# Performance work log

Measured on AMD Instinct MI355X. Metric: run time of the kernel, lower is better.

The kernel has to match this reference:

```python
import jax, jax.numpy as jnp
import numpy as np

B, NA, T, NV, D = 24, 50, 10, 196, 512


def setup_inputs() -> dict:
    key = jax.random.key(0)
    k1, k2 = jax.random.split(key)
    return {
        "audio_feats": jax.random.normal(k1, (B, NA, D), dtype=jnp.float32),
        "visual_feats": jax.random.normal(k2, (B, T, NV, D), dtype=jnp.float32),
        "temperature": jnp.float32(2.5),
        "scale_factor": jnp.float32(2.5),
        "threshold": jnp.float32(-2.5),
    }


def _l2norm(x):
    # F.normalize(dim=-1): x / max(||x||, 1e-12)
    n = jnp.sqrt(jnp.sum(x * x, axis=-1, keepdims=True))
    return x / jnp.maximum(n, 1e-12)


def reference(audio_feats, visual_feats, temperature, scale_factor, threshold):
    b = audio_feats.shape[0]
    a = _l2norm(audio_feats)          # (B,Na,D)
    v = _l2norm(visual_feats)         # (B,T,Nv,D)
    # all-pairs token similarities: (B,B,Na,T,Nv)
    sims = jnp.einsum('xad,ytvd->xyatv', a, v) / temperature

    # aggregate_temporal_similarities
    th = jax.nn.sigmoid(threshold)
    max_vis = jnp.max(sims, axis=-1)            # (B,B,Na,T)
    raw_diff = max_vis - th
    sel = jax.nn.relu(raw_diff) * scale_factor  # selection strength
    weighted_sum = jnp.sum(max_vis * sel, axis=-1)   # over T
    weights_sum = jnp.sum(sel, axis=-1)
    token_sims = weighted_sum / jnp.maximum(weights_sum, 1e-6)
    clip_sims = jnp.mean(token_sims, axis=-1)   # (B,B)
    fraction_selected = jnp.mean((raw_diff > 0).astype(jnp.float32))

    # InfoNCE
    idx = jnp.arange(b)
    losses_a2v = -jax.nn.log_softmax(clip_sims, axis=1)[idx, idx]
    losses_v2a = -jax.nn.log_softmax(clip_sims.T, axis=1)[idx, idx]
    contrastive_loss = jnp.mean(losses_a2v + losses_v2a) / 2

    # regularization
    neg = jnp.clip(sims, -20.0, 0.0)
    l_nonneg = jnp.mean(neg * neg)
    temp_low = jnp.maximum(-jnp.log(temperature), 0.0) ** 2   # log(1)=0
    temp_high = jnp.maximum(jnp.log(temperature) - jnp.log(4.0), 0.0) ** 2
    l_cal = temp_low + temp_high
    l_threshold = jnp.maximum(th - 0.9, 0.0) ** 2 + jnp.maximum(0.1 - th, 0.0) ** 2
    l_scale = jnp.maximum(scale_factor - 20.0, 0.0) ** 2 + jnp.maximum(1.0 - scale_factor, 0.0) ** 2
    reg_loss = 0.15 * l_nonneg + 2.0 * l_cal + 0.1 * l_threshold + 0.1 * l_scale

    # selection reward on positive pairs (diagonal)
    pos_diffs = raw_diff[idx, idx]                       # (B,Na,T)
    sel_ratio = (jnp.tanh(20.0 * pos_diffs) + 1.0) / 2.0
    selection_reward = -0.1 * jnp.log1p(jnp.mean(sel_ratio))

    total_loss = selection_reward + contrastive_loss + reg_loss
    return (total_loss, contrastive_loss, reg_loss, fraction_selected, selection_reward)
```

## Files before the change

### kernel.cpp

```cpp
#include <hip/hip_runtime.h>
#include <math.h>

#define B_   24
#define NA_  50
#define T_   10
#define NV_  196
#define D_   512
#define M_   1200
#define MPAD 1280
#define NVP  224
#define YT_  240
#define VROWS (YT_ * NVP)
#define ABLK 320

#define NT    16
#define BUFB  32768u
#define VBASE 16384u

typedef __bf16 bf16x8 __attribute__((ext_vector_type(8)));
typedef float  f32x4  __attribute__((ext_vector_type(4)));
typedef unsigned short ushort8 __attribute__((ext_vector_type(8)));

__device__ __forceinline__ unsigned short f2bf(float f) {
    unsigned u = __float_as_uint(f);
    u += 0x7FFF + ((u >> 16) & 1);
    return (unsigned short)(u >> 16);
}

__device__ __forceinline__ void gload16(const void* g, void* l) {
    __builtin_amdgcn_global_load_lds(
        (const __attribute__((address_space(1))) unsigned int*)g,
        (__attribute__((address_space(3))) unsigned int*)l, 16, 0, 0);
}

__global__ void normconv_kernel(const float* __restrict__ a,
                                const float* __restrict__ vf,
                                const float* __restrict__ tempPtr,
                                unsigned short* __restrict__ Abf,
                                unsigned short* __restrict__ Vbf,
                                float* __restrict__ accs) {
    if (blockIdx.x == 0 && threadIdx.x < 4) accs[threadIdx.x] = 0.0f;
    int w = threadIdx.x >> 6, lane = threadIdx.x & 63;
    int bid = blockIdx.x;
    const float* src = nullptr;
    ushort8* dst;
    float tscale = 1.0f;
    if (bid < ABLK) {
        int row = bid * 4 + w;
        dst = (ushort8*)(Abf + (size_t)row * D_ + lane * 8);
        if (row < M_) { src = a + (size_t)row * D_ + lane * 8; tscale = tempPtr[0]; }
    } else {
        int row = (bid - ABLK) * 4 + w;
        dst = (ushort8*)(Vbf + (size_t)row * D_ + lane * 8);
        int yt = row / NVP, vv = row - yt * NVP;
        if (vv < NV_) src = vf + ((size_t)yt * NV_ + vv) * D_ + lane * 8;
    }
    if (src) {
        float4 u = *(const float4*)src;
        float4 v = *(const float4*)(src + 4);
        float s = u.x*u.x + u.y*u.y + u.z*u.z + u.w*u.w
                + v.x*v.x + v.y*v.y + v.z*v.z + v.w*v.w;
        #pragma unroll
        for (int off = 32; off; off >>= 1) s += __shfl_xor(s, off, 64);
        float sc = 1.0f / (fmaxf(sqrtf(s), 1e-12f) * tscale);
        ushort8 o;
        o[0]=f2bf(u.x*sc); o[1]=f2bf(u.y*sc); o[2]=f2bf(u.z*sc); o[3]=f2bf(u.w*sc);
        o[4]=f2bf(v.x*sc); o[5]=f2bf(v.y*sc); o[6]=f2bf(v.z*sc); o[7]=f2bf(v.w*sc);
        *dst = o;
    } else {
        ushort8 z = (ushort8)0;
        *dst = z;
    }
}

#define RD_FRAGS(AF, BV, BASE)                                                  \
    _Pragma("unroll") for (int i = 0; i < 4; ++i)                               \
        AF[i] = *(const bf16x8*)((BASE) + aoff[i]);                             \
    _Pragma("unroll") for (int j = 0; j < 7; ++j)                               \
        BV[j] = *(const bf16x8*)((BASE) + boff[j]);

#define MFMA_ALL(AF, BV)                                                        \
    _Pragma("unroll") for (int i = 0; i < 4; ++i)                               \
        _Pragma("unroll") for (int j = 0; j < 7; ++j)                           \
            acc[i][j] = __builtin_amdgcn_mfma_f32_16x16x32_bf16(AF[i], BV[j], acc[i][j], 0, 0, 0);

#define STAGE_T(T, BASEOFF)                                                     \
    _Pragma("unroll") for (int k = 0; k < 4; ++k)                               \
        gload16(gp[k] + (T) * 32, (void*)(lds + (BASEOFF) + loff[k]));

__global__ __launch_bounds__(512, 1) void simred_kernel(
    const unsigned short* __restrict__ Abf, const unsigned short* __restrict__ Vbf,
    float* __restrict__ maxvis, float* __restrict__ accNonneg)
{
    __shared__ __align__(16) unsigned char lds[2 * BUFB];
    float* maxredp = (float*)(lds + 30720);
    float* redbufp = (float*)(lds + BUFB + 30720);

    const int tid  = threadIdx.x;
    const int lane = tid & 63;
    const int w    = tid >> 6;
    const int lrow = lane >> 2;
    const int lcol = lane & 3;
    const int q    = lane >> 4;
    const int m16  = lane & 15;
    const int wr   = w & 3;
    const int wc   = w >> 2;

    const int lin = blockIdx.y * gridDim.x + blockIdx.x;
    const int swz = (lin & 7) * 150 + (lin >> 3);
    const int bx  = swz % 5;
    const int yt  = swz / 5;
    const int rowA0 = bx * 256;
    const size_t vRow0 = (size_t)yt * NVP;

    const int scol = lcol ^ ((lrow >> 1) & 3);
    const unsigned short* gp[4];
    unsigned loff[4];
    #pragma unroll
    for (int k = 0; k < 4; ++k) {
        int u = w + 8 * k;
        if (u < 16)      gp[k] = Abf + ((size_t)(rowA0 + u * 16 + lrow)) * D_ + scol * 8;
        else if (u < 30) gp[k] = Vbf + (vRow0 + (size_t)((u - 16) * 16 + lrow)) * D_ + scol * 8;
        else             gp[k] = Abf + (size_t)lane * 8;
        loff[k] = (unsigned)u * 1024u;
    }

    const unsigned rsw = (unsigned)((m16 >> 1) & 3) * 16u;
    unsigned aoff[4], boff[7];
    #pragma unroll
    for (int i = 0; i < 4; ++i)
        aoff[i] = (unsigned)(wr * 64 + i * 16 + m16) * 64u + (((unsigned)q * 16u) ^ rsw);
    #pragma unroll
    for (int j = 0; j < 7; ++j)
        boff[j] = VBASE + (unsigned)(wc * 112 + j * 16 + m16) * 64u + (((unsigned)q * 16u) ^ rsw);

    f32x4 acc[4][7];
    #pragma unroll
    for (int i = 0; i < 4; ++i)
        #pragma unroll
        for (int j = 0; j < 7; ++j) acc[i][j] = (f32x4)0.0f;

    bf16x8 afA[4], bvA[7], afB[4], bvB[7];

    STAGE_T(0, 0u)
    STAGE_T(1, BUFB)
    asm volatile("s_waitcnt vmcnt(4)\ns_barrier" ::: "memory");
    RD_FRAGS(afA, bvA, lds)

    #pragma unroll
    for (int tp = 0; tp < 8; ++tp) {
        const int t = 2 * tp;
        asm volatile("s_waitcnt vmcnt(0) lgkmcnt(0)\ns_barrier" ::: "memory");
        if (t + 2 < NT) { STAGE_T(t + 2, 0u) }
        RD_FRAGS(afB, bvB, lds + BUFB)
        __builtin_amdgcn_s_setprio(1);
        MFMA_ALL(afA, bvA)
        __builtin_amdgcn_s_setprio(0);
        asm volatile("s_waitcnt vmcnt(0) lgkmcnt(0)\ns_barrier" ::: "memory");
        if (t + 3 < NT) { STAGE_T(t + 3, BUFB) }
        if (t + 2 < NT) { RD_FRAGS(afA, bvA, lds) }
        __builtin_amdgcn_s_setprio(1);
        MFMA_ALL(afB, bvB)
        __builtin_amdgcn_s_setprio(0);
    }

    float cs = 0.0f;
    #pragma unroll
    for (int i = 0; i < 4; ++i)
        #pragma unroll
        for (int j = 0; j < 7; ++j)
            #pragma unroll
            for (int r = 0; r < 4; ++r) {
                float v = acc[i][j][r];
                float cv = fminf(fmaxf(v, -20.0f), 0.0f);
                cs += cv * cv;
            }
    #pragma unroll
    for (int off = 32; off; off >>= 1) cs += __shfl_xor(cs, off, 64);
    if (lane == 0) redbufp[w] = cs;

    bool colv[7];
    #pragma unroll
    for (int j = 0; j < 7; ++j) colv[j] = (wc * 112 + j * 16 + m16) < NV_;
    #pragma unroll
    for (int i = 0; i < 4; ++i) {
        float mx[4] = {-3e38f, -3e38f, -3e38f, -3e38f};
        #pragma unroll
        for (int j = 0; j < 7; ++j)
            #pragma unroll
            for (int r = 0; r < 4; ++r)
                mx[r] = fmaxf(mx[r], colv[j] ? acc[i][j][r] : -3e38f);
        #pragma unroll
        for (int r = 0; r < 4; ++r) {
            float mm = mx[r];
            #pragma unroll
            for (int off = 1; off <= 8; off <<= 1) mm = fmaxf(mm, __shfl_xor(mm, off, 64));
            if (m16 == 0) maxredp[wc * 256 + wr * 64 + i * 16 + q * 4 + r] = mm;
        }
    }
    __syncthreads();
    if (tid == 0) atomicAdd(accNonneg, redbufp[0] + redbufp[1] + redbufp[2] + redbufp[3]
                                     + redbufp[4] + redbufp[5] + redbufp[6] + redbufp[7]);
    if (tid < 256) {
        float mm = fmaxf(maxredp[tid], maxredp[256 + tid]);
        int R = rowA0 + tid;
        if (R < M_) {
            int x = R / NA_, a = R - x * NA_;
            int y = yt / T_, t = yt - y * T_;
            maxvis[(((size_t)x * B_ + y) * NA_ + a) * T_ + t] = mm;
        }
    }
}

__global__ void aggfin_kernel(const float* __restrict__ maxvis,
                              const float* __restrict__ thrPtr,
                              const float* __restrict__ scalePtr,
                              const float* __restrict__ tempPtr,
                              float* __restrict__ clipSims,
                              float* __restrict__ accs,
                              float* __restrict__ out)
{
    int xy = blockIdx.x;
    int x = xy / B_, y = xy % B_;
    int a = threadIdx.x;
    float th    = 1.0f / (1.0f + expf(-thrPtr[0]));
    float scale = scalePtr[0];
    float token = 0.0f, cnt = 0.0f, selsum = 0.0f;
    if (a < NA_) {
        const float* p = maxvis + (((size_t)x * B_ + y) * NA_ + a) * T_;
        float ws = 0.0f, ss = 0.0f;
        #pragma unroll
        for (int t = 0; t < T_; ++t) {
            float mv  = p[t];
            float rd  = mv - th;
            float sel = fmaxf(rd, 0.0f) * scale;
            ws += mv * sel;
            ss += sel;
            if (rd > 0.0f) cnt += 1.0f;
            if (x == y) selsum += 0.5f * (tanhf(20.0f * rd) + 1.0f);
        }
        token = ws / fmaxf(ss, 1e-6f);
    }
    #pragma unroll
    for (int off = 32; off; off >>= 1) {
        token  += __shfl_xor(token,  off, 64);
        cnt    += __shfl_xor(cnt,    off, 64);
        selsum += __shfl_xor(selsum, off, 64);
    }
    if (threadIdx.x == 0) {
        clipSims[x * B_ + y] = token / (float)NA_;
        atomicAdd(&accs[1], cnt);
        if (x == y) atomicAdd(&accs[2], selsum);
    }
    __threadfence();
    unsigned last = 0;
    if (threadIdx.x == 0) {
        unsigned v = atomicAdd((unsigned int*)(accs + 3), 1u);
        last = ((v % (unsigned)(B_ * B_)) == (unsigned)(B_ * B_ - 1));
    }
    last = __shfl((int)last, 0, 64);
    if (!last) return;
    __threadfence();

    __shared__ float cs[B_ * B_];
    int tid = threadIdx.x;
    for (int i = tid; i < B_ * B_; i += 64) cs[i] = clipSims[i];
    __syncthreads();
    float lsum = 0.0f;
    if (tid < B_) {
        int i = tid;
        float m = -1e30f;
        for (int j = 0; j < B_; ++j) m = fmaxf(m, cs[i * B_ + j]);
        float e = 0.0f;
        for (int j = 0; j < B_; ++j) e += expf(cs[i * B_ + j] - m);
        float la = m + logf(e) - cs[i * B_ + i];
        float m2 = -1e30f;
        for (int j = 0; j < B_; ++j) m2 = fmaxf(m2, cs[j * B_ + i]);
        float e2 = 0.0f;
        for (int j = 0; j < B_; ++j) e2 += expf(cs[j * B_ + i] - m2);
        float lv = m2 + logf(e2) - cs[i * B_ + i];
        lsum = la + lv;
    }
    #pragma unroll
    for (int off = 32; off; off >>= 1) lsum += __shfl_xor(lsum, off, 64);
    if (tid == 0) {
        float contrastive = lsum / (float)B_ * 0.5f;
        float temp = tempPtr[0], scl = scalePtr[0];
        float th2 = 1.0f / (1.0f + expf(-thrPtr[0]));
        float l_nonneg = accs[0] / 56448000.0f;
        float logt = logf(temp);
        float tl  = fmaxf(-logt, 0.0f);
        float thi = fmaxf(logt - logf(4.0f), 0.0f);
        float l_cal = tl * tl + thi * thi;
        float t1 = fmaxf(th2 - 0.9f, 0.0f), t2 = fmaxf(0.1f - th2, 0.0f);
        float l_thr = t1 * t1 + t2 * t2;
        float s1 = fmaxf(scl - 20.0f, 0.0f), s2 = fmaxf(1.0f - scl, 0.0f);
        float l_scale = s1 * s1 + s2 * s2;
        float reg = 0.15f * l_nonneg + 2.0f * l_cal + 0.1f * l_thr + 0.1f * l_scale;
        float frac   = accs[1] / 288000.0f;
        float selrew = -0.1f * log1pf(accs[2] / 12000.0f);
        out[0] = selrew + contrastive + reg;
        out[1] = contrastive;
        out[2] = reg;
        out[3] = frac;
        out[4] = selrew;
    }
}

extern "C" void kernel_launch(void* const* d_in, const int* in_sizes, int n_in,
                              void* d_out, int out_size, void* d_ws, size_t ws_size,
                              hipStream_t stream) {
    const float* audio  = (const float*)d_in[0];
    const float* visual = (const float*)d_in[1];
    const float* temp   = (const float*)d_in[2];
    const float* scale  = (const float*)d_in[3];
    const float* thr    = (const float*)d_in[4];
    float* out = (float*)d_out;

    unsigned char* wsb = (unsigned char*)d_ws;
    unsigned short* Abf = (unsigned short*)wsb;
    unsigned short* Vbf = (unsigned short*)(wsb + 1310720);
    float* maxvis   = (float*)(wsb + 1310720 + 55050240);
    float* clipSims = (float*)(wsb + 1310720 + 55050240 + 1152000);
    float* accs     = clipSims + 576;

    normconv_kernel<<<ABLK + VROWS / 4, 256, 0, stream>>>(audio, visual, temp, Abf, Vbf, accs);

    dim3 grid(MPAD / 256, YT_);
    simred_kernel<<<grid, 512, 0, stream>>>(Abf, Vbf, maxvis, accs);

    aggfin_kernel<<<B_ * B_, 64, 0, stream>>>(maxvis, thr, scale, temp, clipSims, accs, out);
}
```

Baseline: 266.8 us.

## Double K-tile depth to 64 and restructure LDS pipeline with XOR swizzle

Each staging step now loads a K-slice of 64 instead of 32, so there are 8 iterations instead of 16, each with two MFMA sub-steps. LDS buffers grow to 64 KB each and use a new 8-way XOR swizzle over 128-byte rows. The register double-buffering of fragments is replaced by reading fragments just before each MFMA batch, which halves the number of barriers but exposes LDS read latency. A barrier is added before the reduction buffer is written because it now overlaps the last-used tile buffer.

Measured after the change: 265.3 us. About the same (-0.6%).

```diff
diff --git a/kernel.cpp b/kernel.cpp
--- a/kernel.cpp
+++ b/kernel.cpp
@@ -13,9 +13,9 @@
 #define VROWS (YT_ * NVP)
 #define ABLK 320
 
-#define NT    16
-#define BUFB  32768u
-#define VBASE 16384u
+#define NT    8
+#define BUFB  65536u
+#define VBASE 32768u
 
 typedef __bf16 bf16x8 __attribute__((ext_vector_type(8)));
 typedef float  f32x4  __attribute__((ext_vector_type(4)));
@@ -73,34 +73,33 @@
     }
 }
 
-#define RD_FRAGS(AF, BV, BASE)                                                  \
+#define STAGE_T(T, BASEOFF)                                                     \
+    _Pragma("unroll") for (int k = 0; k < 8; ++k)                               \
+        gload16(gp[k] + (T) * 64, (void*)(lds + (BASEOFF) + loff[k]));
+
+#define RD_K(BASE, KOFS)                                                        \
     _Pragma("unroll") for (int i = 0; i < 4; ++i)                               \
-        AF[i] = *(const bf16x8*)((BASE) + aoff[i]);                             \
+        af[i] = *(const bf16x8*)((BASE) + (aoff[i] ^ (KOFS)));                  \
     _Pragma("unroll") for (int j = 0; j < 7; ++j)                               \
-        BV[j] = *(const bf16x8*)((BASE) + boff[j]);
-
-#define MFMA_ALL(AF, BV)                                                        \
+        bv[j] = *(const bf16x8*)((BASE) + (boff[j] ^ (KOFS)));
+
+#define MF_ALL()                                                                \
     _Pragma("unroll") for (int i = 0; i < 4; ++i)                               \
         _Pragma("unroll") for (int j = 0; j < 7; ++j)                           \
-            acc[i][j] = __builtin_amdgcn_mfma_f32_16x16x32_bf16(AF[i], BV[j], acc[i][j], 0, 0, 0);
-
-#define STAGE_T(T, BASEOFF)                                                     \
-    _Pragma("unroll") for (int k = 0; k < 4; ++k)                               \
-        gload16(gp[k] + (T) * 32, (void*)(lds + (BASEOFF) + loff[k]));
+            acc[i][j] = __builtin_amdgcn_mfma_f32_16x16x32_bf16(af[i], bv[j], acc[i][j], 0, 0, 0);
 
 __global__ __launch_bounds__(512, 1) void simred_kernel(
     const unsigned short* __restrict__ Abf, const unsigned short* __restrict__ Vbf,
     float* __restrict__ maxvis, float* __restrict__ accNonneg)
 {
     __shared__ __align__(16) unsigned char lds[2 * BUFB];
-    float* maxredp = (float*)(lds + 30720);
-    float* redbufp = (float*)(lds + BUFB + 30720);
+    float* maxredp = (float*)(lds + 61440);
+    float* redbufp = (float*)(lds + BUFB + 61440);
 
     const int tid  = threadIdx.x;
     const int lane = tid & 63;
     const int w    = tid >> 6;
-    const int lrow = lane >> 2;
-    const int lcol = lane & 3;
+    const int lr8  = lane >> 3;
     const int q    = lane >> 4;
     const int m16  = lane & 15;
     const int wr   = w & 3;
@@ -113,26 +112,26 @@
     const int rowA0 = bx * 256;
     const size_t vRow0 = (size_t)yt * NVP;
 
-    const int scol = lcol ^ ((lrow >> 1) & 3);
-    const unsigned short* gp[4];
-    unsigned loff[4];
-    #pragma unroll
-    for (int k = 0; k < 4; ++k) {
+    const int scol = (lane & 7) ^ lr8;
+    const unsigned short* gp[8];
+    unsigned loff[8];
+    #pragma unroll
+    for (int k = 0; k < 8; ++k) {
         int u = w + 8 * k;
-        if (u < 16)      gp[k] = Abf + ((size_t)(rowA0 + u * 16 + lrow)) * D_ + scol * 8;
-        else if (u < 30) gp[k] = Vbf + (vRow0 + (size_t)((u - 16) * 16 + lrow)) * D_ + scol * 8;
+        if (u < 32)      gp[k] = Abf + ((size_t)(rowA0 + u * 8 + lr8)) * D_ + scol * 8;
+        else if (u < 60) gp[k] = Vbf + (vRow0 + (size_t)((u - 32) * 8 + lr8)) * D_ + scol * 8;
         else             gp[k] = Abf + (size_t)lane * 8;
         loff[k] = (unsigned)u * 1024u;
     }
 
-    const unsigned rsw = (unsigned)((m16 >> 1) & 3) * 16u;
+    const unsigned key = (unsigned)(m16 & 7);
     unsigned aoff[4], boff[7];
     #pragma unroll
     for (int i = 0; i < 4; ++i)
-        aoff[i] = (unsigned)(wr * 64 + i * 16 + m16) * 64u + (((unsigned)q * 16u) ^ rsw);
+        aoff[i] = (unsigned)(wr * 64 + i * 16 + m16) * 128u + (((unsigned)q ^ key) * 16u);
     #pragma unroll
     for (int j = 0; j < 7; ++j)
-        boff[j] = VBASE + (unsigned)(wc * 112 + j * 16 + m16) * 64u + (((unsigned)q * 16u) ^ rsw);
+        boff[j] = VBASE + (unsigned)(wc * 112 + j * 16 + m16) * 128u + (((unsigned)q ^ key) * 16u);
 
     f32x4 acc[4][7];
     #pragma unroll
@@ -140,27 +139,19 @@
         #pragma unroll
         for (int j = 0; j < 7; ++j) acc[i][j] = (f32x4)0.0f;
 
-    bf16x8 afA[4], bvA[7], afB[4], bvB[7];
-
     STAGE_T(0, 0u)
-    STAGE_T(1, BUFB)
-    asm volatile("s_waitcnt vmcnt(4)\ns_barrier" ::: "memory");
-    RD_FRAGS(afA, bvA, lds)
-
-    #pragma unroll
-    for (int tp = 0; tp < 8; ++tp) {
-        const int t = 2 * tp;
+
+    #pragma unroll
+    for (int t = 0; t < NT; ++t) {
+        const unsigned char* buf = lds + (unsigned)(t & 1) * BUFB;
         asm volatile("s_waitcnt vmcnt(0) lgkmcnt(0)\ns_barrier" ::: "memory");
-        if (t + 2 < NT) { STAGE_T(t + 2, 0u) }
-        RD_FRAGS(afB, bvB, lds + BUFB)
+        if (t + 1 < NT) { STAGE_T(t + 1, (unsigned)((t + 1) & 1) * BUFB) }
+        bf16x8 af[4], bv[7];
         __builtin_amdgcn_s_setprio(1);
-        MFMA_ALL(afA, bvA)
-        __builtin_amdgcn_s_setprio(0);
-        asm volatile("s_waitcnt vmcnt(0) lgkmcnt(0)\ns_barrier" ::: "memory");
-        if (t + 3 < NT) { STAGE_T(t + 3, BUFB) }
-        if (t + 2 < NT) { RD_FRAGS(afA, bvA, lds) }
-        __builtin_amdgcn_s_setprio(1);
-        MFMA_ALL(afB, bvB)
+        RD_K(buf, 0u)
+        MF_ALL()
+        RD_K(buf, 64u)
+        MF_ALL()
         __builtin_amdgcn_s_setprio(0);
     }
 
@@ -177,6 +168,7 @@
             }
     #pragma unroll
     for (int off = 32; off; off >>= 1) cs += __shfl_xor(cs, off, 64);
+    __syncthreads();
     if (lane == 0) redbufp[w] = cs;
 
     bool colv[7];
```
